# Optimization experiments

Measured on AMD Instinct MI355X. Metric: run time of the kernel, lower is better.

## Reference

```python
import jax, jax.numpy as jnp
import numpy as np

N_ENT = 50000
N_EDGE = 600000
FEAT = 128
HID = 256
OUT = 128
TOTAL_RELS = 2 * 50 + 1  # 2*num_relations + 1
BN_EPS = 1e-5


def setup_inputs() -> dict:
    key = jax.random.key(0)
    ks = jax.random.split(key, 14)

    def xavier(k, shape):
        fan_in, fan_out = shape[0], shape[1]
        bound = float(np.sqrt(6.0 / (fan_in + fan_out)))
        return jax.random.uniform(k, shape, jnp.float32, -bound, bound)

    return {
        "edge_index": jax.random.randint(ks[0], (2, N_EDGE), 0, N_ENT, jnp.int32),
        "edge_type": jax.random.randint(ks[1], (N_EDGE,), 0, TOTAL_RELS, jnp.int32),
        "initial_features": xavier(ks[2], (N_ENT, FEAT)),
        "relation_embeddings": xavier(ks[3], (TOTAL_RELS, FEAT)),
        "W_msg": xavier(ks[4], (FEAT, HID)),
        "b_msg": jnp.zeros((HID,), jnp.float32),
        "W_self": xavier(ks[5], (FEAT, HID)),
        "W1": xavier(ks[6], (HID, HID)),
        "b1": jnp.zeros((HID,), jnp.float32),
        "gamma": jnp.ones((HID,), jnp.float32),
        "beta": jnp.zeros((HID,), jnp.float32),
        "W2": xavier(ks[7], (HID, OUT)),
        "b2": jnp.zeros((OUT,), jnp.float32),
    }


def _forward(edge_index, edge_type, initial_features, relation_embeddings,
             W_msg, b_msg, W_self, W1, b1, gamma, beta, W2, b2):
    x = initial_features                                  # [N, F]
    src, dst = edge_index[0], edge_index[1]

    # Relation-aware message: gather source feature + relation embedding per edge.
    msg = x[src] + relation_embeddings[edge_type]         # [E, F]

    # Degree-normalized scatter aggregation (mean over incoming edges).
    agg = jax.ops.segment_sum(msg, dst, num_segments=N_ENT)           # [N, F]
    deg = jax.ops.segment_sum(jnp.ones((msg.shape[0],), msg.dtype), dst,
                              num_segments=N_ENT)                     # [N]
    agg = agg / jnp.maximum(deg, 1.0)[:, None]

    # RelationGCN layer: transformed aggregate + self-loop path.
    h = agg @ W_msg + x @ W_self + b_msg                  # [N, H]

    # semantic_projector: Linear -> BatchNorm1d (batch stats) -> ReLU -> Linear.
    y = h @ W1 + b1                                       # [N, H]
    mean = jnp.mean(y, axis=0)
    var = jnp.var(y, axis=0)
    y = (y - mean) * jax.lax.rsqrt(var + BN_EPS) * gamma + beta
    y = jax.nn.relu(y)
    # Dropout omitted (deterministic reference).
    out = y @ W2 + b2                                     # [N, O]
    return out


def reference(edge_index, edge_type, initial_features, relation_embeddings,
              W_msg, b_msg, W_self, W1, b1, gamma, beta, W2, b2):
    return _forward(edge_index, edge_type, initial_features, relation_embeddings,
                    W_msg, b_msg, W_self, W1, b1, gamma, beta, W2, b2)
```

## Files before the change

### kernel.cpp

```cpp
#include <hip/hip_runtime.h>
#include <hip/hip_bf16.h>

#define N_ENT   50000
#define N_EDGE  600000
#define FEAT    128
#define HID     256
#define OUT_D   128
#define MROWS   50048
#define BN_EPS  1e-5f
#define SCAN_BLKS 196
#define NT32    (MROWS / 32)
#define RED_BLKS 196

#define OFF_DEGI    0
#define OFF_SCALE   202048
#define OFF_SHIFT   203072
#define OFF_RELB    204096
#define OFF_WT1     229952
#define OFF_W1T     361024
#define OFF_W2T     492096
#define OFF_A       557632
#define OFF_Y       26182208
#define OFF_PB      52000000
#define OFF_PB2     55210000
#define OFF_ROWPTR  56000000
#define OFF_FILLC   56200064
#define OFF_PACKED  56400064
#define OFF_BSUM    58800064

typedef __attribute__((ext_vector_type(8))) short bf16x8;
typedef __attribute__((ext_vector_type(4))) float f32x4;

#define GLL(gp, lp) __builtin_amdgcn_global_load_lds( \
    (const __attribute__((address_space(1))) void*)(gp), \
    (__attribute__((address_space(3))) void*)(lp), 16, 0, 0)

#define MFMA(a, b, c) __builtin_amdgcn_mfma_f32_16x16x32_bf16((a), (b), (c), 0, 0, 0)

__device__ __forceinline__ ushort f2bf(float f) {
    uint u = __float_as_uint(f);
    return (ushort)((u + 0x7FFFu + ((u >> 16) & 1u)) >> 16);
}
__device__ __forceinline__ float bflo(uint u) { return __uint_as_float(u << 16); }
__device__ __forceinline__ float bfhi(uint u) { return __uint_as_float(u & 0xFFFF0000u); }

__global__ __launch_bounds__(256) void k_prep(
    const float* __restrict__ x, const int* __restrict__ ei,
    const float* __restrict__ Wm, const float* __restrict__ Wsf,
    const float* __restrict__ W1, const float* __restrict__ W2,
    const float* __restrict__ rel,
    ushort* __restrict__ A, int* __restrict__ degi,
    ushort* __restrict__ Wt1, ushort* __restrict__ W1t,
    ushort* __restrict__ W2t, ushort* __restrict__ relb)
{
    int b = blockIdx.x;
    if (b < 3125) {
        int idx = b * 256 + threadIdx.x;
        int m = idx >> 4;
        int c = (idx & 15) * 8;
        float4 f0 = *(const float4*)(x + m * FEAT + c);
        float4 f1 = *(const float4*)(x + m * FEAT + c + 4);
        uint4 o;
        o.x = (uint)f2bf(f0.x) | ((uint)f2bf(f0.y) << 16);
        o.y = (uint)f2bf(f0.z) | ((uint)f2bf(f0.w) << 16);
        o.z = (uint)f2bf(f1.x) | ((uint)f2bf(f1.y) << 16);
        o.w = (uint)f2bf(f1.z) | ((uint)f2bf(f1.w) << 16);
        *(uint4*)(A + m * 256 + FEAT + c) = o;
    } else if (b < 3125 + 2344) {
        int e = (b - 3125) * 256 + threadIdx.x;
        if (e < N_EDGE) atomicAdd(&degi[ei[N_EDGE + e]], 1);
    } else {
        int idx = (b - 5469) * 256 + threadIdx.x;
        if (idx < 65536) {
            int n = idx >> 8, k = idx & 255;
            float v = (k < FEAT) ? Wm[k * HID + n] : Wsf[(k - FEAT) * HID + n];
            int w = n >> 6, nb = (n >> 4) & 3, lr = n & 15;
            int kk = k >> 5, lk = (k >> 3) & 3, j = k & 7;
            int l = lk * 16 + lr;
            Wt1[(((w * 8 + kk) * 4 + nb) * 64 + l) * 8 + j] = f2bf(v);
        } else if (idx < 131072) {
            int o = idx - 65536;
            int n = o >> 8, k = o & 255;
            float v = W1[k * HID + n];
            int w = n >> 6, nb = (n >> 4) & 3, lr = n & 15;
            int kk = k >> 5, lk = (k >> 3) & 3, j = k & 7;
            int l = lk * 16 + lr;
            W1t[(((w * 8 + kk) * 4 + nb) * 64 + l) * 8 + j] = f2bf(v);
        } else if (idx < 163840) {
            int o = idx - 131072;
            int n = o >> 8, k = o & 255;
            float v = W2[k * OUT_D + n];
            int w = n >> 5, nb = (n >> 4) & 1, lr = n & 15;
            int kk = k >> 5, lk = (k >> 3) & 3, j = k & 7;
            int l = lk * 16 + lr;
            W2t[(((w * 8 + kk) * 2 + nb) * 64 + l) * 8 + j] = f2bf(v);
        } else if (idx < 163840 + 101 * 128) {
            int o = idx - 163840;
            relb[o] = f2bf(rel[o]);
        }
    }
}

__global__ __launch_bounds__(256) void k_bsum(
    const int* __restrict__ degi, int* __restrict__ bsum)
{
    __shared__ int red[4];
    int idx = blockIdx.x * 256 + threadIdx.x;
    int v = (idx < N_ENT) ? degi[idx] : 0;
    #pragma unroll
    for (int off = 1; off < 64; off <<= 1) v += __shfl_xor(v, off);
    if ((threadIdx.x & 63) == 0) red[threadIdx.x >> 6] = v;
    __syncthreads();
    if (threadIdx.x == 0) bsum[blockIdx.x] = red[0] + red[1] + red[2] + red[3];
}

__global__ __launch_bounds__(256) void k_scan2(
    const int* __restrict__ degi, const int* __restrict__ bsum,
    int* __restrict__ rowptr, int* __restrict__ fillc)
{
    __shared__ int s[256];
    __shared__ int pre[256];
    int t = threadIdx.x;
    pre[t] = (t < blockIdx.x) ? bsum[t] : 0;
    __syncthreads();
    #pragma unroll
    for (int off = 128; off >= 1; off >>= 1) {
        if (t < off) pre[t] += pre[t + off];
        __syncthreads();
    }
    int boff = pre[0];

    int idx = blockIdx.x * 256 + t;
    int v = (idx < N_ENT) ? degi[idx] : 0;
    s[t] = v;
    __syncthreads();
    for (int off = 1; off < 256; off <<= 1) {
        int u = (t >= off) ? s[t - off] : 0;
        __syncthreads();
        s[t] += u;
        __syncthreads();
    }
    if (idx < N_ENT) {
        int ex = s[t] - v + boff;
        rowptr[idx] = ex;
        fillc[idx]  = ex;
    }
    if (blockIdx.x == SCAN_BLKS - 1 && t == 255) rowptr[N_ENT] = boff + s[255];
}

__global__ __launch_bounds__(256) void k_fill(
    const int* __restrict__ ei, const int* __restrict__ et,
    int* __restrict__ fillc, int* __restrict__ packed)
{
    int e = blockIdx.x * 256 + threadIdx.x;
    if (e >= N_EDGE) return;
    int dst = ei[N_EDGE + e];
    int pos = atomicAdd(&fillc[dst], 1);
    packed[pos] = ei[e] | (et[e] << 16);
}

__global__ __launch_bounds__(256) void k_agg(
    const int* __restrict__ rowptr, const int* __restrict__ packed,
    ushort* __restrict__ A, const ushort* __restrict__ relb)
{
    int node = blockIdx.x * 4 + (threadIdx.x >> 6);
    int lane = threadIdx.x & 63;
    int e0 = rowptr[node], e1 = rowptr[node + 1];
    float ax = 0.f, ay = 0.f;
    int e = e0;
    for (; e + 8 <= e1; e += 8) {
        int p0 = packed[e],     p1 = packed[e + 1], p2 = packed[e + 2], p3 = packed[e + 3];
        int p4 = packed[e + 4], p5 = packed[e + 5], p6 = packed[e + 6], p7 = packed[e + 7];
        uint xv0 = *(const uint*)(A + (p0 & 0xFFFF) * 256 + FEAT + lane * 2);
        uint rv0 = *(const uint*)(relb + (p0 >> 16) * FEAT + lane * 2);
        uint xv1 = *(const uint*)(A + (p1 & 0xFFFF) * 256 + FEAT + lane * 2);
        uint rv1 = *(const uint*)(relb + (p1 >> 16) * FEAT + lane * 2);
        uint xv2 = *(const uint*)(A + (p2 & 0xFFFF) * 256 + FEAT + lane * 2);
        uint rv2 = *(const uint*)(relb + (p2 >> 16) * FEAT + lane * 2);
        uint xv3 = *(const uint*)(A + (p3 & 0xFFFF) * 256 + FEAT + lane * 2);
        uint rv3 = *(const uint*)(relb + (p3 >> 16) * FEAT + lane * 2);
        uint xv4 = *(const uint*)(A + (p4 & 0xFFFF) * 256 + FEAT + lane * 2);
        uint rv4 = *(const uint*)(relb + (p4 >> 16) * FEAT + lane * 2);
        uint xv5 = *(const uint*)(A + (p5 & 0xFFFF) * 256 + FEAT + lane * 2);
        uint rv5 = *(const uint*)(relb + (p5 >> 16) * FEAT + lane * 2);
        uint xv6 = *(const uint*)(A + (p6 & 0xFFFF) * 256 + FEAT + lane * 2);
        uint rv6 = *(const uint*)(relb + (p6 >> 16) * FEAT + lane * 2);
        uint xv7 = *(const uint*)(A + (p7 & 0xFFFF) * 256 + FEAT + lane * 2);
        uint rv7 = *(const uint*)(relb + (p7 >> 16) * FEAT + lane * 2);
        ax += bflo(xv0) + bflo(rv0) + bflo(xv1) + bflo(rv1)
            + bflo(xv2) + bflo(rv2) + bflo(xv3) + bflo(rv3)
            + bflo(xv4) + bflo(rv4) + bflo(xv5) + bflo(rv5)
            + bflo(xv6) + bflo(rv6) + bflo(xv7) + bflo(rv7);
        ay += bfhi(xv0) + bfhi(rv0) + bfhi(xv1) + bfhi(rv1)
            + bfhi(xv2) + bfhi(rv2) + bfhi(xv3) + bfhi(rv3)
            + bfhi(xv4) + bfhi(rv4) + bfhi(xv5) + bfhi(rv5)
            + bfhi(xv6) + bfhi(rv6) + bfhi(xv7) + bfhi(rv7);
    }
    for (; e + 4 <= e1; e += 4) {
        int p0 = packed[e], p1 = packed[e + 1], p2 = packed[e + 2], p3 = packed[e + 3];
        uint xv0 = *(const uint*)(A + (p0 & 0xFFFF) * 256 + FEAT + lane * 2);
        uint rv0 = *(const uint*)(relb + (p0 >> 16) * FEAT + lane * 2);
        uint xv1 = *(const uint*)(A + (p1 & 0xFFFF) * 256 + FEAT + lane * 2);
        uint rv1 = *(const uint*)(relb + (p1 >> 16) * FEAT + lane * 2);
        uint xv2 = *(const uint*)(A + (p2 & 0xFFFF) * 256 + FEAT + lane * 2);
        uint rv2 = *(const uint*)(relb + (p2 >> 16) * FEAT + lane * 2);
        uint xv3 = *(const uint*)(A + (p3 & 0xFFFF) * 256 + FEAT + lane * 2);
        uint rv3 = *(const uint*)(relb + (p3 >> 16) * FEAT + lane * 2);
        ax += bflo(xv0) + bflo(rv0) + bflo(xv1) + bflo(rv1)
            + bflo(xv2) + bflo(rv2) + bflo(xv3) + bflo(rv3);
        ay += bfhi(xv0) + bfhi(rv0) + bfhi(xv1) + bfhi(rv1)
            + bfhi(xv2) + bfhi(rv2) + bfhi(xv3) + bfhi(rv3);
    }
    for (; e + 2 <= e1; e += 2) {
        int p0 = packed[e], p1 = packed[e + 1];
        uint xv0 = *(const uint*)(A + (p0 & 0xFFFF) * 256 + FEAT + lane * 2);
        uint rv0 = *(const uint*)(relb + (p0 >> 16) * FEAT + lane * 2);
        uint xv1 = *(const uint*)(A + (p1 & 0xFFFF) * 256 + FEAT + lane * 2);
        uint rv1 = *(const uint*)(relb + (p1 >> 16) * FEAT + lane * 2);
        ax += bflo(xv0) + bflo(rv0) + bflo(xv1) + bflo(rv1);
        ay += bfhi(xv0) + bfhi(rv0) + bfhi(xv1) + bfhi(rv1);
    }
    if (e < e1) {
        int p = packed[e];
        uint xv = *(const uint*)(A + (p & 0xFFFF) * 256 + FEAT + lane * 2);
        uint rv = *(const uint*)(relb + (p >> 16) * FEAT + lane * 2);
        ax += bflo(xv) + bflo(rv);
        ay += bfhi(xv) + bfhi(rv);
    }
    float invd = 1.0f / fmaxf((float)(e1 - e0), 1.0f);
    uint o = (uint)f2bf(ax * invd) | ((uint)f2bf(ay * invd) << 16);
    *(uint*)(A + node * 256 + lane * 2) = o;
}

__global__ __launch_bounds__(256) void k_hy(
    const ushort* __restrict__ A, const ushort* __restrict__ Wt1,
    const ushort* __restrict__ W1t,
    const float* __restrict__ bm, const float* __restrict__ b1,
    ushort* __restrict__ y, float* __restrict__ pb)
{
    __shared__ ushort a_s[32 * 256];
    int tid = threadIdx.x;
    int w = tid >> 6, l = tid & 63;
    int lr = l & 15, lk = l >> 4;
    int m0 = blockIdx.x * 32;

    {
        const ushort* srcb = A + (size_t)m0 * 256;
        #pragma unroll
        for (int j = 0; j < 4; ++j) {
            int slot = (w * 4 + j) * 64 + l;
            int lrow = slot >> 5, lgr = slot & 31;
            GLL(srcb + lrow * 256 + ((lgr ^ (lrow & 7)) << 3), &a_s[(w * 4 + j) * 512]);
        }
    }
    __syncthreads();

    f32x4 acc[2][4] = {};
    const ushort* Bp = Wt1 + w * 16384 + l * 8;
    #pragma unroll
    for (int kk = 0; kk < 8; ++kk) {
        bf16x8 a[2], b[4];
        #pragma unroll
        for (int mb = 0; mb < 2; ++mb) {
            int row = mb * 16 + lr;
            a[mb] = *(const bf16x8*)&a_s[row * 256 + (((kk * 4 + lk) ^ (lr & 7)) << 3)];
        }
        #pragma unroll
        for (int nb = 0; nb < 4; ++nb) b[nb] = *(const bf16x8*)(Bp + kk * 2048 + nb * 512);
        #pragma unroll
        for (int mb = 0; mb < 2; ++mb)
            #pragma unroll
            for (int nb = 0; nb < 4; ++nb)
                acc[mb][nb] = MFMA(a[mb], b[nb], acc[mb][nb]);
    }
    __syncthreads();

    #pragma unroll
    for (int nb = 0; nb < 4; ++nb) {
        int col = w * 64 + nb * 16 + lr;
        float bias = bm[col];
        #pragma unroll
        for (int mb = 0; mb < 2; ++mb)
            #pragma unroll
            for (int r = 0; r < 4; ++r) {
                int row = mb * 16 + lk * 4 + r;
                a_s[row * 256 + (col ^ ((row & 7) << 3))] = f2bf(acc[mb][nb][r] + bias);
            }
    }
    __syncthreads();

    f32x4 acc2[2][4] = {};
    const ushort* B2p = W1t + w * 16384 + l * 8;
    #pragma unroll
    for (int kk = 0; kk < 8; ++kk) {
        bf16x8 a[2], b[4];
        #pragma unroll
        for (int mb = 0; mb < 2; ++mb) {
            int row = mb * 16 + lr;
            a[mb] = *(const bf16x8*)&a_s[row * 256 + ((kk * 32 + lk * 8) ^ ((row & 7) << 3))];
        }
        #pragma unroll
        for (int nb = 0; nb < 4; ++nb) b[nb] = *(const bf16x8*)(B2p + kk * 2048 + nb * 512);
        #pragma unroll
        for (int mb = 0; mb < 2; ++mb)
            #pragma unroll
            for (int nb = 0; nb < 4; ++nb)
                acc2[mb][nb] = MFMA(a[mb], b[nb], acc2[mb][nb]);
    }
    __syncthreads();

    #pragma unroll
    for (int nb = 0; nb < 4; ++nb) {
        int col = w * 64 + nb * 16 + lr;
        float b1v = b1[col];
        float cs = 0.f, cq = 0.f;
        #pragma unroll
        for (int mb = 0; mb < 2; ++mb)
            #pragma unroll
            for (int r = 0; r < 4; ++r) {
                int row = mb * 16 + lk * 4 + r;
                float v = acc2[mb][nb][r] + b1v;
                if (m0 + row < N_ENT) { cs += v; cq += v * v; }
                a_s[row * 256 + (col ^ ((row & 7) << 3))] = f2bf(v);
            }
        cs += __shfl_xor(cs, 16); cs += __shfl_xor(cs, 32);
        cq += __shfl_xor(cq, 16); cq += __shfl_xor(cq, 32);
        if (lk == 0) {
            *(float2*)(pb + (size_t)blockIdx.x * 512 + col * 2) = make_float2(cs, cq);
        }
    }
    __syncthreads();
    ushort* yp = y + (size_t)m0 * 256;
    #pragma unroll
    for (int i = 0; i < 4; ++i) {
        int off = i * 2048 + tid * 8;
        *(uint4*)(yp + off) = *(const uint4*)&a_s[off];
    }
}

__global__ __launch_bounds__(256) void k_red1(
    const float* __restrict__ pb, float* __restrict__ pb2)
{
    int b = blockIdx.x, tid = threadIdx.x;
    int t0 = b * 8;
    float sx = 0.f, sy = 0.f;
    #pragma unroll
    for (int i = 0; i < 8; ++i) {
        int t = t0 + i;
        if (t < NT32) {
            float2 v = *(const float2*)(pb + (size_t)t * 512 + tid * 2);
            sx += v.x; sy += v.y;
        }
    }
    *(float2*)(pb2 + (size_t)b * 512 + tid * 2) = make_float2(sx, sy);
}

__global__ __launch_bounds__(256) void k_red2(
    const float* __restrict__ pb2,
    const float* __restrict__ gamma, const float* __restrict__ beta,
    float* __restrict__ scale, float* __restrict__ shift)
{
    int c = threadIdx.x;
    float s = 0.f, q = 0.f;
    int b = 0;
    #pragma unroll
    for (; b + 8 <= RED_BLKS; b += 8) {
        float2 v0 = *(const float2*)(pb2 + (size_t)(b + 0) * 512 + c * 2);
        float2 v1 = *(const float2*)(pb2 + (size_t)(b + 1) * 512 + c * 2);
        float2 v2 = *(const float2*)(pb2 + (size_t)(b + 2) * 512 + c * 2);
        float2 v3 = *(const float2*)(pb2 + (size_t)(b + 3) * 512 + c * 2);
        float2 v4 = *(const float2*)(pb2 + (size_t)(b + 4) * 512 + c * 2);
        float2 v5 = *(const float2*)(pb2 + (size_t)(b + 5) * 512 + c * 2);
        float2 v6 = *(const float2*)(pb2 + (size_t)(b + 6) * 512 + c * 2);
        float2 v7 = *(const float2*)(pb2 + (size_t)(b + 7) * 512 + c * 2);
        s += v0.x + v1.x + v2.x + v3.x + v4.x + v5.x + v6.x + v7.x;
        q += v0.y + v1.y + v2.y + v3.y + v4.y + v5.y + v6.y + v7.y;
    }
    for (; b < RED_BLKS; ++b) {
        float2 v = *(const float2*)(pb2 + (size_t)b * 512 + c * 2);
        s += v.x; q += v.y;
    }
    const float invn = 1.0f / (float)N_ENT;
    float mean = s * invn;
    float var  = q * invn - mean * mean;
    float rstd = rsqrtf(var + BN_EPS);
    float sc   = gamma[c] * rstd;
    scale[c] = sc;
    shift[c] = beta[c] - mean * sc;
}

__global__ __launch_bounds__(256) void k_zout(
    const ushort* __restrict__ y, const float* __restrict__ scale,
    const float* __restrict__ shift, const ushort* __restrict__ W2t,
    const float* __restrict__ b2, float* __restrict__ out)
{
    __shared__ ushort z_s[32 * 256];
    int tid = threadIdx.x;
    int w = tid >> 6, l = tid & 63;
    int lr = l & 15, lk = l >> 4;
    int m0 = blockIdx.x * 32;

    {
        const ushort* srcb = y + (size_t)m0 * 256;
        #pragma unroll
        for (int j = 0; j < 4; ++j)
            GLL(srcb + ((w * 4 + j) * 64 + l) * 8, &z_s[(w * 4 + j) * 512]);
    }
    __syncthreads();

    f32x4 acc[2][2] = {};
    const ushort* Bp = W2t + w * 8192 + l * 8;
    #pragma unroll
    for (int kk = 0; kk < 8; ++kk) {
        int kb = kk * 32 + lk * 8;
        float scv[8], shv[8];
        *(float4*)&scv[0] = *(const float4*)(scale + kb);
        *(float4*)&scv[4] = *(const float4*)(scale + kb + 4);
        *(float4*)&shv[0] = *(const float4*)(shift + kb);
        *(float4*)&shv[4] = *(const float4*)(shift + kb + 4);
        bf16x8 b[2];
        #pragma unroll
        for (int nb = 0; nb < 2; ++nb) b[nb] = *(const bf16x8*)(Bp + kk * 1024 + nb * 512);
        bf16x8 a[2];
        #pragma unroll
        for (int mb = 0; mb < 2; ++mb) {
            int row = mb * 16 + lr;
            uint4 uv = *(const uint4*)&z_s[row * 256 + (kb ^ ((row & 7) << 3))];
            uint wd[4] = {uv.x, uv.y, uv.z, uv.w};
            #pragma unroll
            for (int j = 0; j < 8; ++j) {
                uint bits = (j & 1) ? (wd[j >> 1] & 0xFFFF0000u) : (wd[j >> 1] << 16);
                float f = __uint_as_float(bits);
                float z = fmaxf(f * scv[j] + shv[j], 0.f);
                a[mb][j] = (short)f2bf(z);
            }
        }
        #pragma unroll
        for (int mb = 0; mb < 2; ++mb)
            #pragma unroll
            for (int nb = 0; nb < 2; ++nb)
                acc[mb][nb] = MFMA(a[mb], b[nb], acc[mb][nb]);
    }
    #pragma unroll
    for (int nb = 0; nb < 2; ++nb) {
        int col = w * 32 + nb * 16 + lr;
        float b2v = b2[col];
        #pragma unroll
        for (int mb = 0; mb < 2; ++mb)
            #pragma unroll
            for (int r = 0; r < 4; ++r) {
                int row = m0 + mb * 16 + lk * 4 + r;
                if (row < N_ENT) out[row * OUT_D + col] = acc[mb][nb][r] + b2v;
            }
    }
}

extern "C" void kernel_launch(void* const* d_in, const int* in_sizes, int n_in,
                              void* d_out, int out_size, void* d_ws, size_t ws_size,
                              hipStream_t stream)
{
    const int*   ei    = (const int*)d_in[0];
    const int*   et    = (const int*)d_in[1];
    const float* x     = (const float*)d_in[2];
    const float* rel   = (const float*)d_in[3];
    const float* Wm    = (const float*)d_in[4];
    const float* bm    = (const float*)d_in[5];
    const float* Wsf   = (const float*)d_in[6];
    const float* W1    = (const float*)d_in[7];
    const float* b1    = (const float*)d_in[8];
    const float* gamma = (const float*)d_in[9];
    const float* beta  = (const float*)d_in[10];
    const float* W2    = (const float*)d_in[11];
    const float* b2    = (const float*)d_in[12];
    float* out = (float*)d_out;

    char* ws = (char*)d_ws;
    int*    degi   = (int*)(ws + OFF_DEGI);
    float*  scale  = (float*)(ws + OFF_SCALE);
    float*  shift  = (float*)(ws + OFF_SHIFT);
    ushort* relb   = (ushort*)(ws + OFF_RELB);
    ushort* Wt1    = (ushort*)(ws + OFF_WT1);
    ushort* W1t    = (ushort*)(ws + OFF_W1T);
    ushort* W2t    = (ushort*)(ws + OFF_W2T);
    ushort* A      = (ushort*)(ws + OFF_A);
    ushort* y      = (ushort*)(ws + OFF_Y);
    int*    rowptr = (int*)(ws + OFF_ROWPTR);
    int*    fillc  = (int*)(ws + OFF_FILLC);
    int*    packed = (int*)(ws + OFF_PACKED);
    int*    bsum   = (int*)(ws + OFF_BSUM);
    float*  pb     = (float*)(ws + OFF_PB);
    float*  pb2    = (float*)(ws + OFF_PB2);

    hipMemsetAsync(ws + OFF_DEGI, 0, 200000, stream);

    k_prep <<<6160, 256, 0, stream>>>(x, ei, Wm, Wsf, W1, W2, rel, A, degi, Wt1, W1t, W2t, relb);
    k_bsum <<<SCAN_BLKS, 256, 0, stream>>>(degi, bsum);
    k_scan2<<<SCAN_BLKS, 256, 0, stream>>>(degi, bsum, rowptr, fillc);
    k_fill <<<(N_EDGE + 255) / 256, 256, 0, stream>>>(ei, et, fillc, packed);
    k_agg  <<<N_ENT / 4, 256, 0, stream>>>(rowptr, packed, A, relb);
    k_hy   <<<NT32, 256, 0, stream>>>(A, Wt1, W1t, bm, b1, y, pb);
    k_red1 <<<RED_BLKS, 256, 0, stream>>>(pb, pb2);
    k_red2 <<<1, 256, 0, stream>>>(pb2, gamma, beta, scale, shift);
    k_zout <<<NT32, 256, 0, stream>>>(y, scale, shift, W2t, b2, out);
}
```

Before: 169.0 us.

## Replace global-atomic CSR build with two-level bucketed counting sort

Builds the destination-sorted edge list with a two-pass bucket sort instead of global atomics. Per-block LDS histograms over 256-node buckets feed a single-block scan. A scatter pass then writes edges into coarse buckets, and a per-bucket kernel does the fine count, scan and placement in shared memory. This removes the memset and the contended global atomics on per-node degree and fill counters. In exchange it adds an intermediate buffer, a serial single-block scan, and bucket blocks whose load depends on how edges are spread.

After: 151.0 us. -10.6%, faster.

```diff
diff --git a/kernel.cpp b/kernel.cpp
--- a/kernel.cpp
+++ b/kernel.cpp
@@ -8,11 +8,12 @@
 #define OUT_D   128
 #define MROWS   50048
 #define BN_EPS  1e-5f
-#define SCAN_BLKS 196
 #define NT32    (MROWS / 32)
 #define RED_BLKS 196
-
-#define OFF_DEGI    0
+#define NBUCK   196
+#define EPB     4096
+#define NBLK_E  147
+
 #define OFF_SCALE   202048
 #define OFF_SHIFT   203072
 #define OFF_RELB    204096
@@ -24,9 +25,11 @@
 #define OFF_PB      52000000
 #define OFF_PB2     55210000
 #define OFF_ROWPTR  56000000
-#define OFF_FILLC   56200064
 #define OFF_PACKED  56400064
-#define OFF_BSUM    58800064
+#define OFF_EBUF    58900000
+#define OFF_CHIST   61300000
+#define OFF_OFFA    61420000
+#define OFF_CBASE   61540000
 
 typedef __attribute__((ext_vector_type(8))) short bf16x8;
 typedef __attribute__((ext_vector_type(4))) float f32x4;
@@ -45,11 +48,11 @@
 __device__ __forceinline__ float bfhi(uint u) { return __uint_as_float(u & 0xFFFF0000u); }
 
 __global__ __launch_bounds__(256) void k_prep(
-    const float* __restrict__ x, const int* __restrict__ ei,
+    const float* __restrict__ x,
     const float* __restrict__ Wm, const float* __restrict__ Wsf,
     const float* __restrict__ W1, const float* __restrict__ W2,
     const float* __restrict__ rel,
-    ushort* __restrict__ A, int* __restrict__ degi,
+    ushort* __restrict__ A,
     ushort* __restrict__ Wt1, ushort* __restrict__ W1t,
     ushort* __restrict__ W2t, ushort* __restrict__ relb)
 {
@@ -66,11 +69,8 @@
         o.z = (uint)f2bf(f1.x) | ((uint)f2bf(f1.y) << 16);
         o.w = (uint)f2bf(f1.z) | ((uint)f2bf(f1.w) << 16);
         *(uint4*)(A + m * 256 + FEAT + c) = o;
-    } else if (b < 3125 + 2344) {
-        int e = (b - 3125) * 256 + threadIdx.x;
-        if (e < N_EDGE) atomicAdd(&degi[ei[N_EDGE + e]], 1);
     } else {
-        int idx = (b - 5469) * 256 + threadIdx.x;
+        int idx = (b - 3125) * 256 + threadIdx.x;
         if (idx < 65536) {
             int n = idx >> 8, k = idx & 255;
             float v = (k < FEAT) ? Wm[k * HID + n] : Wsf[(k - FEAT) * HID + n];
@@ -101,62 +101,102 @@
     }
 }
 
-__global__ __launch_bounds__(256) void k_bsum(
-    const int* __restrict__ degi, int* __restrict__ bsum)
-{
-    __shared__ int red[4];
-    int idx = blockIdx.x * 256 + threadIdx.x;
-    int v = (idx < N_ENT) ? degi[idx] : 0;
-    #pragma unroll
-    for (int off = 1; off < 64; off <<= 1) v += __shfl_xor(v, off);
-    if ((threadIdx.x & 63) == 0) red[threadIdx.x >> 6] = v;
-    __syncthreads();
-    if (threadIdx.x == 0) bsum[blockIdx.x] = red[0] + red[1] + red[2] + red[3];
-}
-
-__global__ __launch_bounds__(256) void k_scan2(
-    const int* __restrict__ degi, const int* __restrict__ bsum,
-    int* __restrict__ rowptr, int* __restrict__ fillc)
+__global__ __launch_bounds__(256) void k_chist(
+    const int* __restrict__ ei, int* __restrict__ chist)
+{
+    __shared__ int h[NBUCK];
+    int t = threadIdx.x;
+    if (t < NBUCK) h[t] = 0;
+    __syncthreads();
+    #pragma unroll
+    for (int r = 0; r < 16; ++r) {
+        int e = (blockIdx.x * 16 + r) * 256 + t;
+        if (e < N_EDGE) atomicAdd(&h[ei[N_EDGE + e] >> 8], 1);
+    }
+    __syncthreads();
+    if (t < NBUCK) chist[blockIdx.x * NBUCK + t] = h[t];
+}
+
+__global__ __launch_bounds__(256) void k_cscan(
+    const int* __restrict__ chist, int* __restrict__ offa, int* __restrict__ cbase)
 {
     __shared__ int s[256];
-    __shared__ int pre[256];
+    int k = threadIdx.x;
+    int acc = 0;
+    if (k < NBUCK) {
+        #pragma unroll 4
+        for (int b = 0; b < NBLK_E; ++b) {
+            offa[b * NBUCK + k] = acc;
+            acc += chist[b * NBUCK + k];
+        }
+    }
+    s[k] = (k < NBUCK) ? acc : 0;
+    int v = s[k];
+    __syncthreads();
+    for (int off = 1; off < 256; off <<= 1) {
+        int u = (k >= off) ? s[k - off] : 0;
+        __syncthreads();
+        s[k] += u;
+        __syncthreads();
+    }
+    if (k < NBUCK) cbase[k] = s[k] - v;
+    if (k == NBUCK - 1) cbase[NBUCK] = s[k];
+}
+
+__global__ __launch_bounds__(256) void k_cscat(
+    const int* __restrict__ ei, const int* __restrict__ et,
+    const int* __restrict__ offa, const int* __restrict__ cbase,
+    int* __restrict__ ebuf)
+{
+    __shared__ int base[NBUCK];
     int t = threadIdx.x;
-    pre[t] = (t < blockIdx.x) ? bsum[t] : 0;
-    __syncthreads();
-    #pragma unroll
-    for (int off = 128; off >= 1; off >>= 1) {
-        if (t < off) pre[t] += pre[t + off];
+    if (t < NBUCK) base[t] = offa[blockIdx.x * NBUCK + t] + cbase[t];
+    __syncthreads();
+    #pragma unroll
+    for (int r = 0; r < 16; ++r) {
+        int e = (blockIdx.x * 16 + r) * 256 + t;
+        if (e < N_EDGE) {
+            int dst = ei[N_EDGE + e];
+            int k = dst >> 8;
+            int pos = atomicAdd(&base[k], 1);
+            ebuf[pos] = ei[e] | (et[e] << 16) | ((dst & 255) << 23);
+        }
+    }
+}
+
+__global__ __launch_bounds__(256) void k_fine(
+    const int* __restrict__ ebuf, const int* __restrict__ cbase,
+    int* __restrict__ rowptr, int* __restrict__ packed)
+{
+    __shared__ int cnt[256], sc[256];
+    int t = threadIdx.x, b = blockIdx.x;
+    int s0 = cbase[b], s1 = cbase[b + 1];
+    cnt[t] = 0;
+    __syncthreads();
+    for (int e = s0 + t; e < s1; e += 256)
+        atomicAdd(&cnt[(ebuf[e] >> 23) & 255], 1);
+    __syncthreads();
+    int v = cnt[t];
+    sc[t] = v;
+    __syncthreads();
+    for (int off = 1; off < 256; off <<= 1) {
+        int u = (t >= off) ? sc[t - off] : 0;
         __syncthreads();
-    }
-    int boff = pre[0];
-
-    int idx = blockIdx.x * 256 + t;
-    int v = (idx < N_ENT) ? degi[idx] : 0;
-    s[t] = v;
-    __syncthreads();
-    for (int off = 1; off < 256; off <<= 1) {
-        int u = (t >= off) ? s[t - off] : 0;
+        sc[t] += u;
         __syncthreads();
-        s[t] += u;
-        __syncthreads();
-    }
-    if (idx < N_ENT) {
-        int ex = s[t] - v + boff;
-        rowptr[idx] = ex;
-        fillc[idx]  = ex;
-    }
-    if (blockIdx.x == SCAN_BLKS - 1 && t == 255) rowptr[N_ENT] = boff + s[255];
-}
-
-__global__ __launch_bounds__(256) void k_fill(
-    const int* __restrict__ ei, const int* __restrict__ et,
-    int* __restrict__ fillc, int* __restrict__ packed)
-{
-    int e = blockIdx.x * 256 + threadIdx.x;
-    if (e >= N_EDGE) return;
-    int dst = ei[N_EDGE + e];
-    int pos = atomicAdd(&fillc[dst], 1);
-    packed[pos] = ei[e] | (et[e] << 16);
+    }
+    int ex = sc[t] - v;
+    int node = b * 256 + t;
+    if (node < N_ENT) rowptr[node] = s0 + ex;
+    if (b == NBUCK - 1 && t == 0) rowptr[N_ENT] = s1;
+    __syncthreads();
+    cnt[t] = s0 + ex;
+    __syncthreads();
+    for (int e = s0 + t; e < s1; e += 256) {
+        int v32 = ebuf[e];
+        int pos = atomicAdd(&cnt[(v32 >> 23) & 255], 1);
+        packed[pos] = v32 & 0x7FFFFF;
+    }
 }
 
 __global__ __launch_bounds__(256) void k_agg(
@@ -475,7 +515,6 @@
     float* out = (float*)d_out;
 
     char* ws = (char*)d_ws;
-    int*    degi   = (int*)(ws + OFF_DEGI);
     float*  scale  = (float*)(ws + OFF_SCALE);
     float*  shift  = (float*)(ws + OFF_SHIFT);
     ushort* relb   = (ushort*)(ws + OFF_RELB);
@@ -484,19 +523,20 @@
     ushort* W2t    = (ushort*)(ws + OFF_W2T);
     ushort* A      = (ushort*)(ws + OFF_A);
     ushort* y      = (ushort*)(ws + OFF_Y);
-    int*    rowptr = (int*)(ws + OFF_ROWPTR);
-    int*    fillc  = (int*)(ws + OFF_FILLC);
-    int*    packed = (int*)(ws + OFF_PACKED);
-    int*    bsum   = (int*)(ws + OFF_BSUM);
     float*  pb     = (float*)(ws + OFF_PB);
     float*  pb2    = (float*)(ws + OFF_PB2);
-
-    hipMemsetAsync(ws + OFF_DEGI, 0, 200000, stream);
-
-    k_prep <<<6160, 256, 0, stream>>>(x, ei, Wm, Wsf, W1, W2, rel, A, degi, Wt1, W1t, W2t, relb);
-    k_bsum <<<SCAN_BLKS, 256, 0, stream>>>(degi, bsum);
-    k_scan2<<<SCAN_BLKS, 256, 0, stream>>>(degi, bsum, rowptr, fillc);
-    k_fill <<<(N_EDGE + 255) / 256, 256, 0, stream>>>(ei, et, fillc, packed);
+    int*    rowptr = (int*)(ws + OFF_ROWPTR);
+    int*    packed = (int*)(ws + OFF_PACKED);
+    int*    ebuf   = (int*)(ws + OFF_EBUF);
+    int*    chist  = (int*)(ws + OFF_CHIST);
+    int*    offa   = (int*)(ws + OFF_OFFA);
+    int*    cbase  = (int*)(ws + OFF_CBASE);
+
+    k_prep <<<3816, 256, 0, stream>>>(x, Wm, Wsf, W1, W2, rel, A, Wt1, W1t, W2t, relb);
+    k_chist<<<NBLK_E, 256, 0, stream>>>(ei, chist);
+    k_cscan<<<1, 256, 0, stream>>>(chist, offa, cbase);
+    k_cscat<<<NBLK_E, 256, 0, stream>>>(ei, et, offa, cbase, ebuf);
+    k_fine <<<NBUCK, 256, 0, stream>>>(ebuf, cbase, rowptr, packed);
     k_agg  <<<N_ENT / 4, 256, 0, stream>>>(rowptr, packed, A, relb);
     k_hy   <<<NT32, 256, 0, stream>>>(A, Wt1, W1t, bm, b1, y, pb);
     k_red1 <<<RED_BLKS, 256, 0, stream>>>(pb, pb2);
```
